# Kernel optimization log

Hardware: AMD Instinct MI355X
Metric: run time of the kernel (lower is better)

The kernel has to match this reference:

```python
import jax, jax.numpy as jnp
import numpy as np

D_MODEL = 1024
N_HEADS = 16


def setup_inputs() -> dict:
    key = jax.random.key(0)
    ks = jax.random.split(key, 11)
    B, L, D = 2, 2048, D_MODEL
    s = 1.0 / np.sqrt(D)
    return {
        "q": jax.random.normal(ks[0], (B, L, D), jnp.float32),
        "k": jax.random.normal(ks[1], (B, L, D), jnp.float32),
        "v": jax.random.normal(ks[2], (B, L, D), jnp.float32),
        "w_q": jax.random.normal(ks[3], (D, D), jnp.float32) * s,
        "b_q": jnp.zeros((D,), jnp.float32),
        "w_k": jax.random.normal(ks[4], (D, D), jnp.float32) * s,
        "b_k": jnp.zeros((D,), jnp.float32),
        "w_v": jax.random.normal(ks[5], (D, D), jnp.float32) * s,
        "b_v": jnp.zeros((D,), jnp.float32),
        "w_o": jax.random.normal(ks[6], (D, D), jnp.float32) * s,
        "b_o": jnp.zeros((D,), jnp.float32),
    }


def reference(q, k, v, w_q, b_q, w_k, b_k, w_v, b_v, w_o, b_o):
    B, L, D = q.shape
    H = N_HEADS
    d_h = D // H
    # QKV projections (nn.Linear: x @ W^T + b)
    qh = (q @ w_q.T + b_q).reshape(B, L, H, d_h).transpose(0, 2, 1, 3)  # [B,H,L,d_h]
    kh = (k @ w_k.T + b_k).reshape(B, L, H, d_h).transpose(0, 2, 1, 3)
    vh = (v @ w_v.T + b_v).reshape(B, L, H, d_h).transpose(0, 2, 1, 3)
    # scaled dot-product attention
    scores = jnp.einsum('bhqd,bhkd->bhqk', qh, kh) / jnp.sqrt(jnp.float32(d_h))
    attn = jax.nn.softmax(scores, axis=-1)                               # [B,H,L,L]
    ctx = jnp.einsum('bhqk,bhkd->bhqd', attn, vh)                        # [B,H,L,d_h]
    ctx = ctx.transpose(0, 2, 1, 3).reshape(B, L, D)
    out = ctx @ w_o.T + b_o
    return out, attn
```

## Files before the change

### kernel.cpp

```cpp
#include <hip/hip_runtime.h>
#include <hip/hip_bf16.h>
#include <stdint.h>

#define DEV static __device__ __forceinline__

typedef float f32x4 __attribute__((ext_vector_type(4)));
typedef __bf16 bf16x8 __attribute__((ext_vector_type(8)));
typedef unsigned short u16x8 __attribute__((ext_vector_type(8)));
typedef unsigned short u16x4 __attribute__((ext_vector_type(4)));
typedef uint32_t u32x2 __attribute__((ext_vector_type(2)));
typedef uint32_t u32x4 __attribute__((ext_vector_type(4)));
typedef unsigned short u16;

#define B_ 2
#define L_ 2048
#define D_MODEL_ 1024
#define H_ 16
#define DH_ 64

#define SHIFT2 11.5415603f

DEV u16 f2bf(float f) {
  union { float f; uint32_t u; } v; v.f = f;
  uint32_t r = v.u + 0x7FFFu + ((v.u >> 16) & 1u);
  return (u16)(r >> 16);
}

DEV float exp2v(float x) {
#if __has_builtin(__builtin_amdgcn_exp2f)
  return __builtin_amdgcn_exp2f(x);
#else
  float r;
  asm("v_exp_f32 %0, %1" : "=v"(r) : "v"(x));
  return r;
#endif
}

DEV uint32_t pkbf(float a, float b) {
  __hip_bfloat162 h = __float22bfloat162_rn(float2{a, b});
  union { __hip_bfloat162 h; uint32_t u; } cv; cv.h = h;
  return cv.u;
}

DEV f32x4 mfma16(bf16x8 a, bf16x8 b, f32x4 c) {
  return __builtin_amdgcn_mfma_f32_16x16x32_bf16(a, b, c, 0, 0, 0);
}

DEV void gl_lds16(const void* g, void* l) {
  __builtin_amdgcn_global_load_lds(
      (const __attribute__((address_space(1))) unsigned int*)g,
      (__attribute__((address_space(3))) unsigned int*)l, 16, 0, 0);
}

struct CastArgs {
  const float* src[8];
  u16* dst[8];
  int n8[8];
};

__global__ __launch_bounds__(256) void cast_kernel(CastArgs a) {
  const int z = blockIdx.z;
  u16* d = a.dst[z];
  const int n8 = a.n8[z];
  const int stride = gridDim.x * blockDim.x;
  if (z == 7) {
    for (int i = blockIdx.x * blockDim.x + threadIdx.x; i < n8; i += stride)
      *((u16x8*)d + i) = u16x8{0, 0, 0, 0, 0, 0, 0, 0};
    return;
  }
  const float* s = a.src[z];
  for (int i = blockIdx.x * blockDim.x + threadIdx.x; i < n8; i += stride) {
    const float4* sp = (const float4*)s + (size_t)i * 2;
    float4 x0 = sp[0], x1 = sp[1];
    u16x8 o;
    o[0] = f2bf(x0.x); o[1] = f2bf(x0.y); o[2] = f2bf(x0.z); o[3] = f2bf(x0.w);
    o[4] = f2bf(x1.x); o[5] = f2bf(x1.y); o[6] = f2bf(x1.z); o[7] = f2bf(x1.w);
    *((u16x8*)d + i) = o;
  }
}

#define GM 4096
#define GN 1024
#define GK 1024

struct GemmArgs {
  const u16* X[3];
  const u16* W[3];
  const float* bias[3];
  void* out[3];
  float alpha[3];
  int mode[3];
};

__global__ __launch_bounds__(256) void gemm_bt(GemmArgs g) {
  const int z = blockIdx.z;
  const u16* X = g.X[z];
  const u16* W = g.W[z];
  const float* bias = g.bias[z];
  const float alpha = g.alpha[z];
  const int mode = g.mode[z];
  const int m0 = blockIdx.y * 128, n0 = blockIdx.x * 128;

  __shared__ __align__(16) char smem[32 * 1024];
  char* As = smem;
  char* Bs = smem + 16 * 1024;

  const int tid = threadIdx.x;
  const int lane = tid & 63, w = tid >> 6;
  const int l15 = lane & 15, l4 = lane >> 4;
  const int wm = (w >> 1) * 64, wn = (w & 1) * 64;

  f32x4 acc[4][4];
#pragma unroll
  for (int i = 0; i < 4; ++i)
#pragma unroll
    for (int j = 0; j < 4; ++j) acc[i][j] = f32x4{0.f, 0.f, 0.f, 0.f};

  for (int ks = 0; ks < GK; ks += 64) {
    __syncthreads();
    for (int c = w; c < 16; c += 4) {
      int r = c * 8 + (lane >> 3);
      int j = lane & 7;
      int sj = j ^ (r & 7);
      gl_lds16((const char*)(X + (size_t)(m0 + r) * GK + ks) + sj * 16, As + c * 1024);
      gl_lds16((const char*)(W + (size_t)(n0 + r) * GK + ks) + sj * 16, Bs + c * 1024);
    }
    __syncthreads();
#pragma unroll
    for (int ksub = 0; ksub < 2; ++ksub) {
      bf16x8 af[4], bfr[4];
#pragma unroll
      for (int mf = 0; mf < 4; ++mf) {
        int r = wm + mf * 16 + l15;
        int j16 = ksub * 4 + l4;
        af[mf] = *(const bf16x8*)(As + r * 128 + ((j16 ^ (r & 7)) * 16));
      }
#pragma unroll
      for (int nf = 0; nf < 4; ++nf) {
        int r = wn + nf * 16 + l15;
        int j16 = ksub * 4 + l4;
        bfr[nf] = *(const bf16x8*)(Bs + r * 128 + ((j16 ^ (r & 7)) * 16));
      }
#pragma unroll
      for (int mf = 0; mf < 4; ++mf)
#pragma unroll
        for (int nf = 0; nf < 4; ++nf) acc[mf][nf] = mfma16(af[mf], bfr[nf], acc[mf][nf]);
    }
  }

  if (mode == 2) {
    u16* base = (u16*)g.out[z];
#pragma unroll
    for (int nf = 0; nf < 4; ++nf) {
      int n = n0 + wn + nf * 16 + l15;
      float bv = bias[n];
#pragma unroll
      for (int mf = 0; mf < 4; ++mf) {
        int m = m0 + wm + mf * 16 + l4 * 4;
        u16x4 pk;
#pragma unroll
        for (int r = 0; r < 4; ++r) pk[r] = f2bf((acc[mf][nf][r] + bv) * alpha);
        size_t off = (((size_t)(m >> 11) * H_ + (n >> 6)) * DH_ + (n & 63)) * (size_t)L_ + (m & 2047);
        *(u16x4*)(base + off) = pk;
      }
    }
  } else {
#pragma unroll
    for (int nf = 0; nf < 4; ++nf) {
      int n = n0 + wn + nf * 16 + l15;
      float bv = bias[n];
#pragma unroll
      for (int mf = 0; mf < 4; ++mf) {
#pragma unroll
        for (int r = 0; r < 4; ++r) {
          int m = m0 + wm + mf * 16 + l4 * 4 + r;
          float val = (acc[mf][nf][r] + bv) * alpha;
          if (mode == 1)
            ((float*)g.out[z])[(size_t)m * GN + n] = val;
          else
            ((u16*)g.out[z])[(size_t)m * GN + n] = f2bf(val);
        }
      }
    }
  }
}

__global__ __launch_bounds__(256) void sumexp_kernel(const u16* Qp, const u16* Kp,
                                                     float* sums) {
  const int q0 = blockIdx.x * 64;
  const int kc0 = blockIdx.y * 512;
  const int bh = blockIdx.z;
  const int b = bh >> 4, h = bh & 15;
  const int tid = threadIdx.x, lane = tid & 63, w = tid >> 6;
  const int l15 = lane & 15, l4 = lane >> 4;
  const int lr = lane >> 3, lj = lane & 7;

  __shared__ __align__(16) char smem[16 * 1024];

  const u16* Qbase = Qp + ((size_t)(b * L_ + q0 + w * 16) * D_MODEL_ + h * DH_);
  const u16* Kbase = Kp + ((size_t)(b * L_ + kc0) * D_MODEL_ + h * DH_);

  auto stK = [&](int t) {
    const int c0 = t * 64, bsel = (t & 1) << 13;
    for (int c = w; c < 8; c += 4) {
      int r = c * 8 + lr, sj = lj ^ (r & 7);
      gl_lds16((const char*)(Kbase + (size_t)(c0 + r) * D_MODEL_) + sj * 16,
               smem + bsel + c * 1024);
    }
  };

  bf16x8 qa[2];
#pragma unroll
  for (int ksub = 0; ksub < 2; ++ksub)
    qa[ksub] = *(const bf16x8*)(Qbase + (size_t)l15 * D_MODEL_ + (ksub * 4 + l4) * 8);

  stK(0);
  __syncthreads();

  float ssum = 0.f;
  for (int t = 0; t < 8; ++t) {
    if (t < 7) stK(t + 1);
    const char* Ks = smem + ((t & 1) << 13);
    f32x4 s[4];
#pragma unroll
    for (int nf = 0; nf < 4; ++nf) s[nf] = f32x4{0.f, 0.f, 0.f, 0.f};
#pragma unroll
    for (int ksub = 0; ksub < 2; ++ksub) {
      int j16 = ksub * 4 + l4;
      bf16x8 kb[4];
#pragma unroll
      for (int nf = 0; nf < 4; ++nf) {
        int r = nf * 16 + l15;
        kb[nf] = *(const bf16x8*)(Ks + r * 128 + ((j16 ^ (r & 7)) * 16));
      }
#pragma unroll
      for (int nf = 0; nf < 4; ++nf) s[nf] = mfma16(kb[nf], qa[ksub], s[nf]);
    }
#pragma unroll
    for (int nf = 0; nf < 4; ++nf)
#pragma unroll
      for (int r = 0; r < 4; ++r) ssum += exp2v(s[nf][r] - SHIFT2);
    __syncthreads();
  }

  ssum += __shfl_xor(ssum, 16);
  ssum += __shfl_xor(ssum, 32);
  if (lane < 16)
    atomicAdd(&sums[((size_t)bh << 11) + q0 + w * 16 + lane], ssum);
}

__global__ __launch_bounds__(256) void attn_kernel(const u16* Qp, const u16* Kp,
                                                   const u16* VT, const float* sums,
                                                   float* attn, u16* ctx) {
  const int q0 = blockIdx.x * 64;
  const int h = blockIdx.y, b = blockIdx.z;
  const int tid = threadIdx.x, lane = tid & 63, w = tid >> 6;
  const int l15 = lane & 15, l4 = lane >> 4;
  const int lr = lane >> 3, lj = lane & 7;

  __shared__ __align__(16) char smem[32 * 1024];
  char* Pw = smem + w * 4096;

  const u16* Qbase = Qp + ((size_t)(b * L_ + q0 + w * 16) * D_MODEL_ + h * DH_);
  const u16* Kbase = Kp + ((size_t)(b * L_) * D_MODEL_ + h * DH_);
  const u16* Vb = VT + ((size_t)((b * H_ + h) * DH_) * L_);
  float* attnb = attn + ((size_t)(b * H_ + h)) * L_ * L_;

  auto stK = [&](int t) {
    const int c0 = t * 64, bsel = (t & 1) << 13;
    for (int c = w; c < 8; c += 4) {
      int r = c * 8 + lr, sj = lj ^ (r & 7);
      gl_lds16((const char*)(Kbase + (size_t)(c0 + r) * D_MODEL_) + sj * 16,
               smem + 16384 + bsel + c * 1024);
    }
  };

  bf16x8 qa[2];
#pragma unroll
  for (int ksub = 0; ksub < 2; ++ksub)
    qa[ksub] = *(const bf16x8*)(Qbase + (size_t)l15 * D_MODEL_ + (ksub * 4 + l4) * 8);

  const float c2 =
      SHIFT2 + __log2f(sums[(((size_t)(b * H_ + h)) << 11) + q0 + w * 16 + l15]);

  stK(0);

  f32x4 cacc[4];
#pragma unroll
  for (int i = 0; i < 4; ++i) cacc[i] = f32x4{0.f, 0.f, 0.f, 0.f};

  const int swz = l15 & 7;
  float* awave = attnb + (size_t)(q0 + w * 16) * L_;
  __syncthreads();

  for (int t = 0; t < 32; ++t) {
    const int c0 = t * 64;
    if (t < 31) stK(t + 1);
    bf16x8 va[2][4];
#pragma unroll
    for (int ksub = 0; ksub < 2; ++ksub)
#pragma unroll
      for (int df = 0; df < 4; ++df)
        va[ksub][df] = *(const bf16x8*)(Vb + (size_t)(df * 16 + l15) * L_ + c0 +
                                        (ksub * 4 + l4) * 8);
    __builtin_amdgcn_sched_barrier(0);

    const char* Ks = smem + 16384 + ((t & 1) << 13);
    f32x4 s[4];
#pragma unroll
    for (int nf = 0; nf < 4; ++nf) s[nf] = f32x4{0.f, 0.f, 0.f, 0.f};
    __builtin_amdgcn_s_setprio(1);
#pragma unroll
    for (int ksub = 0; ksub < 2; ++ksub) {
      int j16 = ksub * 4 + l4;
      bf16x8 kb[4];
#pragma unroll
      for (int nf = 0; nf < 4; ++nf) {
        int r = nf * 16 + l15;
        kb[nf] = *(const bf16x8*)(Ks + r * 128 + ((j16 ^ (r & 7)) * 16));
      }
#pragma unroll
      for (int nf = 0; nf < 4; ++nf) s[nf] = mfma16(kb[nf], qa[ksub], s[nf]);
    }
    __builtin_amdgcn_s_setprio(0);

#pragma unroll
    for (int nf = 0; nf < 4; ++nf) {
      f32x4 p4;
#pragma unroll
      for (int r = 0; r < 4; ++r) p4[r] = exp2v(s[nf][r] - c2);
      *(f32x4*)(Pw + l15 * 256 + (((nf * 4 + l4) ^ swz) * 16)) = p4;
    }
#pragma unroll
    for (int j = 0; j < 4; ++j) {
      int row = 4 * j + (lane >> 4);
      f32x4 v = *(const f32x4*)(Pw + row * 256 + (((lane & 15) ^ (row & 7)) * 16));
      __builtin_nontemporal_store(
          v, (f32x4*)(awave + (size_t)row * L_ + c0 + (lane & 15) * 4));
    }
    __builtin_amdgcn_s_setprio(1);
#pragma unroll
    for (int ksub = 0; ksub < 2; ++ksub) {
      int cbase = (ksub * 4 + l4) * 2;
      f32x4 plo = *(const f32x4*)(Pw + l15 * 256 + ((cbase ^ swz) * 16));
      f32x4 phi = *(const f32x4*)(Pw + l15 * 256 + (((cbase + 1) ^ swz) * 16));
      union { u32x4 u; bf16x8 h; } pa;
      pa.u[0] = pkbf(plo[0], plo[1]);
      pa.u[1] = pkbf(plo[2], plo[3]);
      pa.u[2] = pkbf(phi[0], phi[1]);
      pa.u[3] = pkbf(phi[2], phi[3]);
#pragma unroll
      for (int df = 0; df < 4; ++df)
        cacc[df] = mfma16(pa.h, va[ksub][df], cacc[df]);
    }
    __builtin_amdgcn_s_setprio(0);
    if (t < 31) {
      asm volatile("s_waitcnt vmcnt(12)" ::: "memory");
      __builtin_amdgcn_s_barrier();
      __builtin_amdgcn_sched_barrier(0);
    }
  }

#pragma unroll
  for (int df = 0; df < 4; ++df) {
#pragma unroll
    for (int r = 0; r < 4; ++r) {
      int row = q0 + w * 16 + l4 * 4 + r;
      int col = h * DH_ + df * 16 + l15;
      ctx[(size_t)(b * L_ + row) * D_MODEL_ + col] = f2bf(cacc[df][r]);
    }
  }
}

extern "C" void kernel_launch(void* const* d_in, const int* in_sizes, int n_in,
                              void* d_out, int out_size, void* d_ws, size_t ws_size,
                              hipStream_t stream) {
  const float* q = (const float*)d_in[0];
  const float* k = (const float*)d_in[1];
  const float* v = (const float*)d_in[2];
  const float* w_q = (const float*)d_in[3];
  const float* b_q = (const float*)d_in[4];
  const float* w_k = (const float*)d_in[5];
  const float* b_k = (const float*)d_in[6];
  const float* w_v = (const float*)d_in[7];
  const float* b_v = (const float*)d_in[8];
  const float* w_o = (const float*)d_in[9];
  const float* b_o = (const float*)d_in[10];

  float* out = (float*)d_out;
  float* attn = (float*)d_out + (size_t)B_ * L_ * D_MODEL_;

  const size_t MB = 1u << 20;
  char* ws = (char*)d_ws;
  u16* qb = (u16*)(ws + 0 * MB);
  u16* kb = (u16*)(ws + 8 * MB);
  u16* vb = (u16*)(ws + 16 * MB);
  u16* wqb = (u16*)(ws + 24 * MB);
  u16* wkb = (u16*)(ws + 26 * MB);
  u16* wvb = (u16*)(ws + 28 * MB);
  u16* wob = (u16*)(ws + 30 * MB);
  u16* Qp = (u16*)(ws + 32 * MB);
  u16* Kp = (u16*)(ws + 40 * MB);
  u16* VT = (u16*)(ws + 48 * MB);
  float* sums = (float*)(ws + 56 * MB);
  u16* ctx = kb;

  CastArgs ca;
  ca.src[0] = q;   ca.dst[0] = qb;  ca.n8[0] = (B_ * L_ * D_MODEL_) / 8;
  ca.src[1] = k;   ca.dst[1] = kb;  ca.n8[1] = (B_ * L_ * D_MODEL_) / 8;
  ca.src[2] = v;   ca.dst[2] = vb;  ca.n8[2] = (B_ * L_ * D_MODEL_) / 8;
  ca.src[3] = w_q; ca.dst[3] = wqb; ca.n8[3] = (D_MODEL_ * D_MODEL_) / 8;
  ca.src[4] = w_k; ca.dst[4] = wkb; ca.n8[4] = (D_MODEL_ * D_MODEL_) / 8;
  ca.src[5] = w_v; ca.dst[5] = wvb; ca.n8[5] = (D_MODEL_ * D_MODEL_) / 8;
  ca.src[6] = w_o; ca.dst[6] = wob; ca.n8[6] = (D_MODEL_ * D_MODEL_) / 8;
  ca.src[7] = nullptr; ca.dst[7] = (u16*)sums; ca.n8[7] = (B_ * H_ * L_ * 4) / 16;
  cast_kernel<<<dim3(1024, 1, 8), 256, 0, stream>>>(ca);

  GemmArgs ga;
  ga.X[0] = qb;  ga.W[0] = wqb; ga.bias[0] = b_q; ga.out[0] = Qp; ga.alpha[0] = 0.125f * 1.44269504f; ga.mode[0] = 0;
  ga.X[1] = kb;  ga.W[1] = wkb; ga.bias[1] = b_k; ga.out[1] = Kp; ga.alpha[1] = 1.f;    ga.mode[1] = 0;
  ga.X[2] = vb;  ga.W[2] = wvb; ga.bias[2] = b_v; ga.out[2] = VT; ga.alpha[2] = 1.f;    ga.mode[2] = 2;
  gemm_bt<<<dim3(8, 32, 3), 256, 0, stream>>>(ga);

  sumexp_kernel<<<dim3(32, 4, 32), 256, 0, stream>>>(Qp, Kp, sums);

  attn_kernel<<<dim3(32, 16, 2), 256, 0, stream>>>(Qp, Kp, VT, sums, attn, ctx);

  GemmArgs go;
  go.X[0] = ctx; go.W[0] = wob; go.bias[0] = b_o; go.out[0] = out; go.alpha[0] = 1.f; go.mode[0] = 1;
  go.X[1] = ctx; go.W[1] = wob; go.bias[1] = b_o; go.out[1] = out; go.alpha[1] = 1.f; go.mode[1] = 1;
  go.X[2] = ctx; go.W[2] = wob; go.bias[2] = b_o; go.out[2] = out; go.alpha[2] = 1.f; go.mode[2] = 1;
  gemm_bt<<<dim3(8, 32, 1), 256, 0, stream>>>(go);
}
```

Measured before the change: 276.2 us.

## Split attention key range across two blocks with atomic fp32 context reduction

Doubles the attention grid by having each block handle half of the key sequence, so twice as many workgroups run over the CUs. Partial context results are accumulated with fp32 atomicAdd into a zeroed workspace buffer, then a new conversion kernel casts that buffer to bf16 for the output projection. This adds a 16MB zero-fill, atomic traffic and an extra kernel launch. It also drops the per-block pipeline from 32 to 16 tiles, leaving fewer tiles to hide load latency.

```diff
diff --git a/kernel.cpp b/kernel.cpp
--- a/kernel.cpp
+++ b/kernel.cpp
@@ -53,9 +53,9 @@
 }
 
 struct CastArgs {
-  const float* src[8];
-  u16* dst[8];
-  int n8[8];
+  const float* src[9];
+  u16* dst[9];
+  int n8[9];
 };
 
 __global__ __launch_bounds__(256) void cast_kernel(CastArgs a) {
@@ -63,12 +63,12 @@
   u16* d = a.dst[z];
   const int n8 = a.n8[z];
   const int stride = gridDim.x * blockDim.x;
-  if (z == 7) {
+  const float* s = a.src[z];
+  if (s == nullptr) {
     for (int i = blockIdx.x * blockDim.x + threadIdx.x; i < n8; i += stride)
       *((u16x8*)d + i) = u16x8{0, 0, 0, 0, 0, 0, 0, 0};
     return;
   }
-  const float* s = a.src[z];
   for (int i = blockIdx.x * blockDim.x + threadIdx.x; i < n8; i += stride) {
     const float4* sp = (const float4*)s + (size_t)i * 2;
     float4 x0 = sp[0], x1 = sp[1];
@@ -77,6 +77,16 @@
     o[4] = f2bf(x1.x); o[5] = f2bf(x1.y); o[6] = f2bf(x1.z); o[7] = f2bf(x1.w);
     *((u16x8*)d + i) = o;
   }
+}
+
+__global__ __launch_bounds__(256) void ctxcvt_kernel(const float* cf, u16* cb) {
+  const int i = blockIdx.x * blockDim.x + threadIdx.x;
+  const f32x4* p = (const f32x4*)cf + (size_t)i * 2;
+  f32x4 a = p[0], b = p[1];
+  u16x8 o;
+  o[0] = f2bf(a[0]); o[1] = f2bf(a[1]); o[2] = f2bf(a[2]); o[3] = f2bf(a[3]);
+  o[4] = f2bf(b[0]); o[5] = f2bf(b[1]); o[6] = f2bf(b[2]); o[7] = f2bf(b[3]);
+  *((u16x8*)cb + i) = o;
 }
 
 #define GM 4096
@@ -251,9 +261,11 @@
 
 __global__ __launch_bounds__(256) void attn_kernel(const u16* Qp, const u16* Kp,
                                                    const u16* VT, const float* sums,
-                                                   float* attn, u16* ctx) {
+                                                   float* attn, float* ctxf) {
   const int q0 = blockIdx.x * 64;
-  const int h = blockIdx.y, b = blockIdx.z;
+  const int h = blockIdx.y;
+  const int b = blockIdx.z >> 1;
+  const int kc0 = (blockIdx.z & 1) * 1024;
   const int tid = threadIdx.x, lane = tid & 63, w = tid >> 6;
   const int l15 = lane & 15, l4 = lane >> 4;
   const int lr = lane >> 3, lj = lane & 7;
@@ -262,9 +274,9 @@
   char* Pw = smem + w * 4096;
 
   const u16* Qbase = Qp + ((size_t)(b * L_ + q0 + w * 16) * D_MODEL_ + h * DH_);
-  const u16* Kbase = Kp + ((size_t)(b * L_) * D_MODEL_ + h * DH_);
-  const u16* Vb = VT + ((size_t)((b * H_ + h) * DH_) * L_);
-  float* attnb = attn + ((size_t)(b * H_ + h)) * L_ * L_;
+  const u16* Kbase = Kp + ((size_t)(b * L_ + kc0) * D_MODEL_ + h * DH_);
+  const u16* Vb = VT + ((size_t)((b * H_ + h) * DH_) * L_) + kc0;
+  float* attnb = attn + ((size_t)(b * H_ + h)) * L_ * L_ + kc0;
 
   auto stK = [&](int t) {
     const int c0 = t * 64, bsel = (t & 1) << 13;
@@ -293,9 +305,9 @@
   float* awave = attnb + (size_t)(q0 + w * 16) * L_;
   __syncthreads();
 
-  for (int t = 0; t < 32; ++t) {
+  for (int t = 0; t < 16; ++t) {
     const int c0 = t * 64;
-    if (t < 31) stK(t + 1);
+    if (t < 15) stK(t + 1);
     bf16x8 va[2][4];
 #pragma unroll
     for (int ksub = 0; ksub < 2; ++ksub)
@@ -354,7 +366,7 @@
         cacc[df] = mfma16(pa.h, va[ksub][df], cacc[df]);
     }
     __builtin_amdgcn_s_setprio(0);
-    if (t < 31) {
+    if (t < 15) {
       asm volatile("s_waitcnt vmcnt(12)" ::: "memory");
       __builtin_amdgcn_s_barrier();
       __builtin_amdgcn_sched_barrier(0);
@@ -367,7 +379,7 @@
     for (int r = 0; r < 4; ++r) {
       int row = q0 + w * 16 + l4 * 4 + r;
       int col = h * DH_ + df * 16 + l15;
-      ctx[(size_t)(b * L_ + row) * D_MODEL_ + col] = f2bf(cacc[df][r]);
+      atomicAdd(&ctxf[(size_t)(b * L_ + row) * D_MODEL_ + col], cacc[df][r]);
     }
   }
 }
@@ -403,6 +415,7 @@
   u16* Kp = (u16*)(ws + 40 * MB);
   u16* VT = (u16*)(ws + 48 * MB);
   float* sums = (float*)(ws + 56 * MB);
+  float* ctxf = (float*)(ws + 58 * MB);
   u16* ctx = kb;
 
   CastArgs ca;
@@ -414,7 +427,8 @@
   ca.src[5] = w_v; ca.dst[5] = wvb; ca.n8[5] = (D_MODEL_ * D_MODEL_) / 8;
   ca.src[6] = w_o; ca.dst[6] = wob; ca.n8[6] = (D_MODEL_ * D_MODEL_) / 8;
   ca.src[7] = nullptr; ca.dst[7] = (u16*)sums; ca.n8[7] = (B_ * H_ * L_ * 4) / 16;
-  cast_kernel<<<dim3(1024, 1, 8), 256, 0, stream>>>(ca);
+  ca.src[8] = nullptr; ca.dst[8] = (u16*)ctxf; ca.n8[8] = (B_ * L_ * D_MODEL_ * 4) / 16;
+  cast_kernel<<<dim3(1024, 1, 9), 256, 0, stream>>>(ca);
 
   GemmArgs ga;
   ga.X[0] = qb;  ga.W[0] = wqb; ga.bias[0] = b_q; ga.out[0] = Qp; ga.alpha[0] = 0.125f * 1.44269504f; ga.mode[0] = 0;
@@ -424,7 +438,9 @@
 
   sumexp_kernel<<<dim3(32, 4, 32), 256, 0, stream>>>(Qp, Kp, sums);
 
-  attn_kernel<<<dim3(32, 16, 2), 256, 0, stream>>>(Qp, Kp, VT, sums, attn, ctx);
+  attn_kernel<<<dim3(32, 16, 4), 256, 0, stream>>>(Qp, Kp, VT, sums, attn, ctxf);
+
+  ctxcvt_kernel<<<dim3((B_ * L_ * D_MODEL_) / 8 / 256, 1, 1), 256, 0, stream>>>(ctxf, ctx);
 
   GemmArgs go;
   go.X[0] = ctx; go.W[0] = wob; go.bias[0] = b_o; go.out[0] = out; go.alpha[0] = 1.f; go.mode[0] = 1;
```

After: 281.5 us. Within noise of the previous version (+1.9%).

## Stage V tiles through double-buffered LDS via async loads in attention kernel

Applied to the files above, without the earlier changes.

The attention kernel now stages the transposed V tile for each key block into a double-buffered LDS region using global_load_lds, the same way K is staged. Previously each wave read V straight from global memory into registers. The vmcnt wait threshold is changed to account for the different number of outstanding loads. The attention-probability stores switch from nontemporal to regular stores, and the cast kernel's zero-fill branch now tests for a null source pointer instead of z==7. LDS use grows from 32 KB to 48 KB, which may lower occupancy.

```diff
diff --git a/kernel.cpp b/kernel.cpp
--- a/kernel.cpp
+++ b/kernel.cpp
@@ -63,12 +63,12 @@
   u16* d = a.dst[z];
   const int n8 = a.n8[z];
   const int stride = gridDim.x * blockDim.x;
-  if (z == 7) {
+  const float* s = a.src[z];
+  if (s == nullptr) {
     for (int i = blockIdx.x * blockDim.x + threadIdx.x; i < n8; i += stride)
       *((u16x8*)d + i) = u16x8{0, 0, 0, 0, 0, 0, 0, 0};
     return;
   }
-  const float* s = a.src[z];
   for (int i = blockIdx.x * blockDim.x + threadIdx.x; i < n8; i += stride) {
     const float4* sp = (const float4*)s + (size_t)i * 2;
     float4 x0 = sp[0], x1 = sp[1];
@@ -258,12 +258,12 @@
   const int l15 = lane & 15, l4 = lane >> 4;
   const int lr = lane >> 3, lj = lane & 7;
 
-  __shared__ __align__(16) char smem[32 * 1024];
+  __shared__ __align__(16) char smem[48 * 1024];
   char* Pw = smem + w * 4096;
 
   const u16* Qbase = Qp + ((size_t)(b * L_ + q0 + w * 16) * D_MODEL_ + h * DH_);
   const u16* Kbase = Kp + ((size_t)(b * L_) * D_MODEL_ + h * DH_);
-  const u16* Vb = VT + ((size_t)((b * H_ + h) * DH_) * L_);
+  const u16* VTb = VT + ((size_t)((b * H_ + h) * DH_) * L_);
   float* attnb = attn + ((size_t)(b * H_ + h)) * L_ * L_;
 
   auto stK = [&](int t) {
@@ -274,6 +274,14 @@
                smem + 16384 + bsel + c * 1024);
     }
   };
+  auto stV = [&](int t) {
+    const int c0 = t * 64, bsel = (t & 1) << 13;
+    for (int c = w; c < 8; c += 4) {
+      int r = c * 8 + lr, sj = lj ^ (r & 7);
+      gl_lds16((const char*)(VTb + (size_t)r * L_ + c0) + sj * 16,
+               smem + 32768 + bsel + c * 1024);
+    }
+  };
 
   bf16x8 qa[2];
 #pragma unroll
@@ -284,6 +292,7 @@
       SHIFT2 + __log2f(sums[(((size_t)(b * H_ + h)) << 11) + q0 + w * 16 + l15]);
 
   stK(0);
+  stV(0);
 
   f32x4 cacc[4];
 #pragma unroll
@@ -295,17 +304,11 @@
 
   for (int t = 0; t < 32; ++t) {
     const int c0 = t * 64;
-    if (t < 31) stK(t + 1);
-    bf16x8 va[2][4];
-#pragma unroll
-    for (int ksub = 0; ksub < 2; ++ksub)
-#pragma unroll
-      for (int df = 0; df < 4; ++df)
-        va[ksub][df] = *(const bf16x8*)(Vb + (size_t)(df * 16 + l15) * L_ + c0 +
-                                        (ksub * 4 + l4) * 8);
+    if (t < 31) { stK(t + 1); stV(t + 1); }
     __builtin_amdgcn_sched_barrier(0);
 
     const char* Ks = smem + 16384 + ((t & 1) << 13);
+    const char* Vs = smem + 32768 + ((t & 1) << 13);
     f32x4 s[4];
 #pragma unroll
     for (int nf = 0; nf < 4; ++nf) s[nf] = f32x4{0.f, 0.f, 0.f, 0.f};
@@ -335,8 +338,7 @@
     for (int j = 0; j < 4; ++j) {
       int row = 4 * j + (lane >> 4);
       f32x4 v = *(const f32x4*)(Pw + row * 256 + (((lane & 15) ^ (row & 7)) * 16));
-      __builtin_nontemporal_store(
-          v, (f32x4*)(awave + (size_t)row * L_ + c0 + (lane & 15) * 4));
+      *(f32x4*)(awave + (size_t)row * L_ + c0 + (lane & 15) * 4) = v;
     }
     __builtin_amdgcn_s_setprio(1);
 #pragma unroll
@@ -349,13 +351,17 @@
       pa.u[1] = pkbf(plo[2], plo[3]);
       pa.u[2] = pkbf(phi[0], phi[1]);
       pa.u[3] = pkbf(phi[2], phi[3]);
-#pragma unroll
-      for (int df = 0; df < 4; ++df)
-        cacc[df] = mfma16(pa.h, va[ksub][df], cacc[df]);
+      int j16 = ksub * 4 + l4;
+#pragma unroll
+      for (int df = 0; df < 4; ++df) {
+        int r = df * 16 + l15;
+        bf16x8 vb = *(const bf16x8*)(Vs + r * 128 + ((j16 ^ (r & 7)) * 16));
+        cacc[df] = mfma16(pa.h, vb, cacc[df]);
+      }
     }
     __builtin_amdgcn_s_setprio(0);
     if (t < 31) {
-      asm volatile("s_waitcnt vmcnt(12)" ::: "memory");
+      asm volatile("s_waitcnt vmcnt(4)" ::: "memory");
       __builtin_amdgcn_s_barrier();
       __builtin_amdgcn_sched_barrier(0);
     }
```

Result: slower. 290.2 us (+5.1%).

## Split attention kernel into independent single-wave blocks without barriers

Applied to the files above, without the earlier changes.

The attention kernel now launches one 64-thread wave per block, covering 16 query rows, instead of four waves sharing a double-buffered K tile. Each wave loads its own K tiles into LDS, so all block barriers and the explicit vmcnt wait are gone. The QK^T MFMA for the current tile is moved ahead of issuing the next K prefetch and the V loads. The attention-probability stores change from nontemporal to ordinary stores. The aim is to remove barrier stalls and give the scheduler more independent waves, at the cost of four times the K global-to-LDS traffic per query block and different cache behaviour for the large attn output.

```diff
diff --git a/kernel.cpp b/kernel.cpp
--- a/kernel.cpp
+++ b/kernel.cpp
@@ -8,7 +8,6 @@
 typedef __bf16 bf16x8 __attribute__((ext_vector_type(8)));
 typedef unsigned short u16x8 __attribute__((ext_vector_type(8)));
 typedef unsigned short u16x4 __attribute__((ext_vector_type(4)));
-typedef uint32_t u32x2 __attribute__((ext_vector_type(2)));
 typedef uint32_t u32x4 __attribute__((ext_vector_type(4)));
 typedef unsigned short u16;
 
@@ -63,12 +62,12 @@
   u16* d = a.dst[z];
   const int n8 = a.n8[z];
   const int stride = gridDim.x * blockDim.x;
-  if (z == 7) {
+  const float* s = a.src[z];
+  if (s == nullptr) {
     for (int i = blockIdx.x * blockDim.x + threadIdx.x; i < n8; i += stride)
       *((u16x8*)d + i) = u16x8{0, 0, 0, 0, 0, 0, 0, 0};
     return;
   }
-  const float* s = a.src[z];
   for (int i = blockIdx.x * blockDim.x + threadIdx.x; i < n8; i += stride) {
     const float4* sp = (const float4*)s + (size_t)i * 2;
     float4 x0 = sp[0], x1 = sp[1];
@@ -249,29 +248,30 @@
     atomicAdd(&sums[((size_t)bh << 11) + q0 + w * 16 + lane], ssum);
 }
 
-__global__ __launch_bounds__(256) void attn_kernel(const u16* Qp, const u16* Kp,
-                                                   const u16* VT, const float* sums,
-                                                   float* attn, u16* ctx) {
-  const int q0 = blockIdx.x * 64;
+__global__ __launch_bounds__(64) void attn_kernel(const u16* Qp, const u16* Kp,
+                                                  const u16* VT, const float* sums,
+                                                  float* attn, u16* ctx) {
+  const int q0 = blockIdx.x * 16;
   const int h = blockIdx.y, b = blockIdx.z;
-  const int tid = threadIdx.x, lane = tid & 63, w = tid >> 6;
+  const int lane = threadIdx.x & 63;
   const int l15 = lane & 15, l4 = lane >> 4;
   const int lr = lane >> 3, lj = lane & 7;
 
-  __shared__ __align__(16) char smem[32 * 1024];
-  char* Pw = smem + w * 4096;
-
-  const u16* Qbase = Qp + ((size_t)(b * L_ + q0 + w * 16) * D_MODEL_ + h * DH_);
+  __shared__ __align__(16) char smem[20 * 1024];
+  char* Pw = smem + 16384;
+
+  const u16* Qbase = Qp + ((size_t)(b * L_ + q0) * D_MODEL_ + h * DH_);
   const u16* Kbase = Kp + ((size_t)(b * L_) * D_MODEL_ + h * DH_);
   const u16* Vb = VT + ((size_t)((b * H_ + h) * DH_) * L_);
   float* attnb = attn + ((size_t)(b * H_ + h)) * L_ * L_;
 
   auto stK = [&](int t) {
     const int c0 = t * 64, bsel = (t & 1) << 13;
-    for (int c = w; c < 8; c += 4) {
+#pragma unroll
+    for (int c = 0; c < 8; ++c) {
       int r = c * 8 + lr, sj = lj ^ (r & 7);
       gl_lds16((const char*)(Kbase + (size_t)(c0 + r) * D_MODEL_) + sj * 16,
-               smem + 16384 + bsel + c * 1024);
+               smem + bsel + c * 1024);
     }
   };
 
@@ -281,7 +281,7 @@
     qa[ksub] = *(const bf16x8*)(Qbase + (size_t)l15 * D_MODEL_ + (ksub * 4 + l4) * 8);
 
   const float c2 =
-      SHIFT2 + __log2f(sums[(((size_t)(b * H_ + h)) << 11) + q0 + w * 16 + l15]);
+      SHIFT2 + __log2f(sums[(((size_t)(b * H_ + h)) << 11) + q0 + l15]);
 
   stK(0);
 
@@ -290,11 +290,29 @@
   for (int i = 0; i < 4; ++i) cacc[i] = f32x4{0.f, 0.f, 0.f, 0.f};
 
   const int swz = l15 & 7;
-  float* awave = attnb + (size_t)(q0 + w * 16) * L_;
-  __syncthreads();
 
   for (int t = 0; t < 32; ++t) {
     const int c0 = t * 64;
+    const char* Ks = smem + ((t & 1) << 13);
+
+    f32x4 s[4];
+#pragma unroll
+    for (int nf = 0; nf < 4; ++nf) s[nf] = f32x4{0.f, 0.f, 0.f, 0.f};
+    __builtin_amdgcn_s_setprio(1);
+#pragma unroll
+    for (int ksub = 0; ksub < 2; ++ksub) {
+      int j16 = ksub * 4 + l4;
+      bf16x8 kb[4];
+#pragma unroll
+      for (int nf = 0; nf < 4; ++nf) {
+        int r = nf * 16 + l15;
+        kb[nf] = *(const bf16x8*)(Ks + r * 128 + ((j16 ^ (r & 7)) * 16));
+      }
+#pragma unroll
+      for (int nf = 0; nf < 4; ++nf) s[nf] = mfma16(kb[nf], qa[ksub], s[nf]);
+    }
+    __builtin_amdgcn_s_setprio(0);
+
     if (t < 31) stK(t + 1);
     bf16x8 va[2][4];
 #pragma unroll
@@ -303,26 +321,6 @@
       for (int df = 0; df < 4; ++df)
         va[ksub][df] = *(const bf16x8*)(Vb + (size_t)(df * 16 + l15) * L_ + c0 +
                                         (ksub * 4 + l4) * 8);
-    __builtin_amdgcn_sched_barrier(0);
-
-    const char* Ks = smem + 16384 + ((t & 1) << 13);
-    f32x4 s[4];
-#pragma unroll
-    for (int nf = 0; nf < 4; ++nf) s[nf] = f32x4{0.f, 0.f, 0.f, 0.f};
-    __builtin_amdgcn_s_setprio(1);
-#pragma unroll
-    for (int ksub = 0; ksub < 2; ++ksub) {
-      int j16 = ksub * 4 + l4;
-      bf16x8 kb[4];
-#pragma unroll
-      for (int nf = 0; nf < 4; ++nf) {
-        int r = nf * 16 + l15;
-        kb[nf] = *(const bf16x8*)(Ks + r * 128 + ((j16 ^ (r & 7)) * 16));
-      }
-#pragma unroll
-      for (int nf = 0; nf < 4; ++nf) s[nf] = mfma16(kb[nf], qa[ksub], s[nf]);
-    }
-    __builtin_amdgcn_s_setprio(0);
 
 #pragma unroll
     for (int nf = 0; nf < 4; ++nf) {
@@ -331,12 +329,12 @@
       for (int r = 0; r < 4; ++r) p4[r] = exp2v(s[nf][r] - c2);
       *(f32x4*)(Pw + l15 * 256 + (((nf * 4 + l4) ^ swz) * 16)) = p4;
     }
+    float* awave = attnb + (size_t)q0 * L_ + c0;
 #pragma unroll
     for (int j = 0; j < 4; ++j) {
       int row = 4 * j + (lane >> 4);
       f32x4 v = *(const f32x4*)(Pw + row * 256 + (((lane & 15) ^ (row & 7)) * 16));
-      __builtin_nontemporal_store(
-          v, (f32x4*)(awave + (size_t)row * L_ + c0 + (lane & 15) * 4));
+      *(f32x4*)(awave + (size_t)row * L_ + (lane & 15) * 4) = v;
     }
     __builtin_amdgcn_s_setprio(1);
 #pragma unroll
@@ -354,18 +352,13 @@
         cacc[df] = mfma16(pa.h, va[ksub][df], cacc[df]);
     }
     __builtin_amdgcn_s_setprio(0);
-    if (t < 31) {
-      asm volatile("s_waitcnt vmcnt(12)" ::: "memory");
-      __builtin_amdgcn_s_barrier();
-      __builtin_amdgcn_sched_barrier(0);
-    }
   }
 
 #pragma unroll
   for (int df = 0; df < 4; ++df) {
 #pragma unroll
     for (int r = 0; r < 4; ++r) {
-      int row = q0 + w * 16 + l4 * 4 + r;
+      int row = q0 + l4 * 4 + r;
       int col = h * DH_ + df * 16 + l15;
       ctx[(size_t)(b * L_ + row) * D_MODEL_ + col] = f2bf(cacc[df][r]);
     }
@@ -424,7 +417,7 @@
 
   sumexp_kernel<<<dim3(32, 4, 32), 256, 0, stream>>>(Qp, Kp, sums);
 
-  attn_kernel<<<dim3(32, 16, 2), 256, 0, stream>>>(Qp, Kp, VT, sums, attn, ctx);
+  attn_kernel<<<dim3(128, 16, 2), 64, 0, stream>>>(Qp, Kp, VT, sums, attn, ctx);
 
   GemmArgs go;
   go.X[0] = ctx; go.W[0] = wob; go.bias[0] = b_o; go.out[0] = out; go.alpha[0] = 1.f; go.mode[0] = 1;
```

Measured after the change: 341.4 us. +23.6%, slower.
